# Kernel optimization log

Measured on AMD Instinct MI355X. Metric: run time of the kernel, lower is better.

Reference implementation:

```python
import jax, jax.numpy as jnp
import numpy as np

NODES_PER_GRAPH = 64
HIDDEN = 128
NUM_LAYERS = 4
NUM_CLASSES = 32
EPS = 1e-5


def fully_adjacent_edges(n, num_batches):
    # block-diagonal fully connected edges: within each graph, all (src, dst) pairs
    offs = jnp.arange(num_batches, dtype=jnp.int32) * n          # [G]
    a = jnp.arange(n, dtype=jnp.int32)
    src = jnp.broadcast_to(offs[:, None, None] + a[None, :, None], (num_batches, n, n)).reshape(-1)
    dst = jnp.broadcast_to(offs[:, None, None] + a[None, None, :], (num_batches, n, n)).reshape(-1)
    return jnp.stack([src, dst])  # [2, G*n*n]


def gcn_conv(h, edge_index, W, b, num_nodes):
    loops = jnp.arange(num_nodes, dtype=edge_index.dtype)
    src = jnp.concatenate([edge_index[0], loops])
    dst = jnp.concatenate([edge_index[1], loops])
    deg = jax.ops.segment_sum(jnp.ones_like(dst, dtype=h.dtype), dst, num_segments=num_nodes)
    dinv = jnp.where(deg > 0, jax.lax.rsqrt(deg), 0.0)
    hw = h @ W                                         # [N, H]
    norm = dinv[src] * dinv[dst]                       # [E+N]
    msg = hw[src] * norm[:, None]                      # [E+N, H] (dominant traffic)
    return jax.ops.segment_sum(msg, dst, num_segments=num_nodes) + b


def layer_norm(h, g, b):
    mu = jnp.mean(h, axis=-1, keepdims=True)
    var = jnp.mean(jnp.square(h - mu), axis=-1, keepdims=True)
    return (h - mu) * jax.lax.rsqrt(var + EPS) * g + b


def setup_inputs() -> dict:
    key = jax.random.key(0)
    ks = jax.random.split(key, 8)
    G, n = 256, NODES_PER_GRAPH
    N = G * n
    E = 262144
    x = jax.random.randint(ks[0], (N, 2), 0, NUM_CLASSES, dtype=jnp.int32)
    edge_index = jax.random.randint(ks[1], (2, E), 0, N, dtype=jnp.int32)
    batch = (jnp.arange(N, dtype=jnp.int32) // n).astype(jnp.int32)
    s = 1.0 / np.sqrt(HIDDEN)
    return {
        "x": x,
        "edge_index": edge_index,
        "batch": batch,
        "class_emb": jax.random.normal(ks[2], (NUM_CLASSES, HIDDEN), jnp.float32) * 0.02,
        "neigh_emb": jax.random.normal(ks[3], (NUM_CLASSES, HIDDEN), jnp.float32) * 0.02,
        "Ws": jax.random.normal(ks[4], (NUM_LAYERS, HIDDEN, HIDDEN), jnp.float32) * s,
        "bs": jnp.zeros((NUM_LAYERS, HIDDEN), jnp.float32),
        "ln_g": jnp.ones((NUM_LAYERS, HIDDEN), jnp.float32),
        "ln_b": jnp.zeros((NUM_LAYERS, HIDDEN), jnp.float32),
        "out_W": jax.random.normal(ks[5], (HIDDEN, NUM_CLASSES), jnp.float32) * s,
        "out_b": jnp.zeros((NUM_CLASSES,), jnp.float32),
    }


def reference(x, edge_index, batch, class_emb, neigh_emb, Ws, bs, ln_g, ln_b, out_W, out_b):
    N = x.shape[0]
    G = N // NODES_PER_GRAPH
    h = class_emb[x[:, 0]] + neigh_emb[x[:, 1]]          # embedding sum  [N, H]
    fa_edges = fully_adjacent_edges(NODES_PER_GRAPH, G)  # use_fully_adj=True -> last layer
    for i in range(NUM_LAYERS):
        ei = fa_edges if (i + 1 == NUM_LAYERS) else edge_index
        h_new = jax.nn.relu(gcn_conv(h, ei, Ws[i], bs[i], N))
        h = layer_norm(h + h_new, ln_g[i], ln_b[i])
    roots = jnp.arange(G) * NODES_PER_GRAPH              # root_mask: node 0 of each graph
    return h[roots] @ out_W + out_b                      # [G, NUM_CLASSES]
```

## Files before the change

kernel.cpp:

```cpp
#include <hip/hip_runtime.h>

#define NN 16384
#define EE 262144
#define HH 128
#define GG 256
#define NPG 64
#define ELLW 64

__global__ __launch_bounds__(256) void k_ell(const int* __restrict__ ei,
                                             int* __restrict__ cnt, int* __restrict__ col) {
  int e = blockIdx.x * 256 + threadIdx.x;
  int d = ei[EE + e];
  int s = atomicAdd(&cnt[d], 1);
  if (s < ELLW) col[d * ELLW + s] = ei[e];
}

__device__ __forceinline__ void gemm32(const float (*Al)[132], float* Wl,
                                       const float* __restrict__ W, float* __restrict__ C,
                                       int rbase, int tid) {
  int cg = (tid & 31) * 4;
  int rg = (tid >> 5) * 2;
  float acc[2][4];
#pragma unroll
  for (int i = 0; i < 2; ++i)
#pragma unroll
    for (int j = 0; j < 4; ++j) acc[i][j] = 0.f;
  for (int kc = 0; kc < 4; ++kc) {
    int k0 = kc * 32;
#pragma unroll
    for (int i = 0; i < 2; ++i) {
      int f = tid + 512 * i;
      int kk = f >> 5, q = f & 31;
      *(float4*)&Wl[kk * 128 + q * 4] = *(const float4*)&W[(k0 + kk) * HH + q * 4];
    }
    __syncthreads();
#pragma unroll
    for (int kk = 0; kk < 32; kk += 4) {
      float av[2][4], wv_[4][4];
#pragma unroll
      for (int i = 0; i < 2; ++i) *(float4*)av[i] = *(const float4*)&Al[rg + i][k0 + kk];
#pragma unroll
      for (int j = 0; j < 4; ++j) *(float4*)wv_[j] = *(const float4*)&Wl[(kk + j) * 128 + cg];
#pragma unroll
      for (int j = 0; j < 4; ++j)
#pragma unroll
        for (int i = 0; i < 2; ++i)
#pragma unroll
          for (int c = 0; c < 4; ++c) acc[i][c] = fmaf(av[i][j], wv_[j][c], acc[i][c]);
    }
    __syncthreads();
  }
#pragma unroll
  for (int i = 0; i < 2; ++i) {
    float4 o; o.x = acc[i][0]; o.y = acc[i][1]; o.z = acc[i][2]; o.w = acc[i][3];
    *(float4*)&C[(rbase + rg + i) * HH + cg] = o;
  }
}

__global__ __launch_bounds__(512) void k_emb_gemm(const int* __restrict__ x,
    const float* __restrict__ ce, const float* __restrict__ ne, const float* __restrict__ W,
    const int* __restrict__ cnt, float* __restrict__ h, float* __restrict__ hw,
    float* __restrict__ dinv) {
  __shared__ __align__(16) float Wl[32 * 128];
  __shared__ __align__(16) float Al[32][132];
  int tid = threadIdx.x;
  int rbase = blockIdx.x * 32;
#pragma unroll
  for (int u = 0; u < 2; ++u) {
    int idx = tid + 512 * u;
    int r = idx >> 5, q = idx & 31;
    int2 cls = ((const int2*)x)[rbase + r];
    float4 a = ((const float4*)ce)[cls.x * 32 + q];
    float4 b = ((const float4*)ne)[cls.y * 32 + q];
    float4 o; o.x = a.x + b.x; o.y = a.y + b.y; o.z = a.z + b.z; o.w = a.w + b.w;
    *(float4*)&Al[r][q * 4] = o;
    ((float4*)h)[(rbase + r) * 32 + q] = o;
  }
  if (tid < 32) dinv[rbase + tid] = rsqrtf((float)(cnt[rbase + tid] + 1));
  gemm32(Al, Wl, W, hw, rbase, tid);
}

__global__ __launch_bounds__(512) void k_agg_gemm(const float* __restrict__ hwin,
    float* __restrict__ h, const int* __restrict__ col, const int* __restrict__ cnt,
    const float* __restrict__ dinv, const float* __restrict__ bias,
    const float* __restrict__ g, const float* __restrict__ bln,
    const float* __restrict__ W, float* __restrict__ hwout) {
  __shared__ __align__(16) float Wl[32 * 128];
  __shared__ __align__(16) float Al[32][132];
  int tid = threadIdx.x, wv = tid >> 6, lane = tid & 63;
  int rbase = blockIdx.x * 32;
  const float2* hw2 = (const float2*)hwin;
  float2* h2 = (float2*)h;
  int d = lane * 2;
  float2 b2 = *(const float2*)&bias[d];
  float2 gg = *(const float2*)&g[d];
  float2 bb = *(const float2*)&bln[d];
#pragma unroll 1
  for (int i = 0; i < 4; ++i) {
    int n = rbase + wv * 4 + i;
    float dn = dinv[n];
    float2 sv = hw2[n * 64 + lane];
    float a0x = sv.x * dn * dn, a0y = sv.y * dn * dn;
    float a1x = 0.f, a1y = 0.f, a2x = 0.f, a2y = 0.f, a3x = 0.f, a3y = 0.f;
    int m = cnt[n]; m = m > ELLW ? ELLW : m;
    int cl = 0; float dv = 0.f;
    if (lane < m) { cl = col[n * ELLW + lane]; dv = dinv[cl]; }
    int j = 0;
    for (; j + 4 <= m; j += 4) {
      int s0 = __shfl(cl, j),     s1 = __shfl(cl, j + 1);
      int s2 = __shfl(cl, j + 2), s3 = __shfl(cl, j + 3);
      float n0 = __shfl(dv, j) * dn,     n1 = __shfl(dv, j + 1) * dn;
      float n2 = __shfl(dv, j + 2) * dn, n3 = __shfl(dv, j + 3) * dn;
      float2 v0 = hw2[s0 * 64 + lane];
      float2 v1 = hw2[s1 * 64 + lane];
      float2 v2 = hw2[s2 * 64 + lane];
      float2 v3 = hw2[s3 * 64 + lane];
      a0x = fmaf(v0.x, n0, a0x); a0y = fmaf(v0.y, n0, a0y);
      a1x = fmaf(v1.x, n1, a1x); a1y = fmaf(v1.y, n1, a1y);
      a2x = fmaf(v2.x, n2, a2x); a2y = fmaf(v2.y, n2, a2y);
      a3x = fmaf(v3.x, n3, a3x); a3y = fmaf(v3.y, n3, a3y);
    }
    for (; j < m; ++j) {
      int s0 = __shfl(cl, j); float n0 = __shfl(dv, j) * dn;
      float2 v0 = hw2[s0 * 64 + lane];
      a0x = fmaf(v0.x, n0, a0x); a0y = fmaf(v0.y, n0, a0y);
    }
    float accx = (a0x + a1x) + (a2x + a3x);
    float accy = (a0y + a1y) + (a2y + a3y);
    float hnx = fmaxf(accx + b2.x, 0.f), hny = fmaxf(accy + b2.y, 0.f);
    float2 hv = h2[n * 64 + lane];
    float rx = hv.x + hnx, ry = hv.y + hny;
    float s1 = rx + ry, s2 = rx * rx + ry * ry;
#pragma unroll
    for (int o = 1; o < 64; o <<= 1) { s1 += __shfl_xor(s1, o); s2 += __shfl_xor(s2, o); }
    float mu = s1 * (1.f / 128.f);
    float var = s2 * (1.f / 128.f) - mu * mu;
    float rstd = rsqrtf(var + 1e-5f);
    float2 o2;
    o2.x = (rx - mu) * rstd * gg.x + bb.x;
    o2.y = (ry - mu) * rstd * gg.y + bb.y;
    h2[n * 64 + lane] = o2;
    *(float2*)&Al[wv * 4 + i][2 * lane] = o2;
  }
  gemm32(Al, Wl, W, hwout, rbase, tid);
}

__global__ __launch_bounds__(256) void k_fa_out(const float* __restrict__ hw, float* __restrict__ h,
    const float* __restrict__ bias, const float* __restrict__ g, const float* __restrict__ bln,
    const float* __restrict__ oW, const float* __restrict__ ob, float* __restrict__ out) {
  __shared__ float tmp[256];
  __shared__ float gsum[128];
  __shared__ float part[8][32];
  int gph = blockIdx.x;
  int tid = threadIdx.x;
  int d = tid & 127, half = tid >> 7;
  const float* hwbase = hw + gph * NPG * HH;
  float s = 0.f;
#pragma unroll
  for (int r = 0; r < 32; ++r) s += hwbase[(half * 32 + r) * HH + d];
  tmp[tid] = s;
  __syncthreads();
  if (tid < 128) gsum[tid] = tmp[tid] + tmp[tid + 128];
  __syncthreads();
  int wv = tid >> 6, lane = tid & 63;
  const float inv65 = 1.0f / 65.0f;
  float2 gs = *(const float2*)&gsum[lane * 2];
  float2 b2 = *(const float2*)&bias[lane * 2];
  float2 gg = *(const float2*)&g[lane * 2];
  float2 bb = *(const float2*)&bln[lane * 2];
  __syncthreads();
  for (int ni = wv; ni < NPG; ni += 4) {
    int n = gph * NPG + ni;
    float2 hwv = ((const float2*)hw)[n * 64 + lane];
    float ax = fmaxf((gs.x + hwv.x) * inv65 + b2.x, 0.f);
    float ay = fmaxf((gs.y + hwv.y) * inv65 + b2.y, 0.f);
    float2 hv = ((float2*)h)[n * 64 + lane];
    float rx = hv.x + ax, ry = hv.y + ay;
    float s1 = rx + ry, s2 = rx * rx + ry * ry;
#pragma unroll
    for (int o = 1; o < 64; o <<= 1) { s1 += __shfl_xor(s1, o); s2 += __shfl_xor(s2, o); }
    float mu = s1 * (1.f / 128.f);
    float var = s2 * (1.f / 128.f) - mu * mu;
    float rstd = rsqrtf(var + 1e-5f);
    float2 o2;
    o2.x = (rx - mu) * rstd * gg.x + bb.x;
    o2.y = (ry - mu) * rstd * gg.y + bb.y;
    if (ni == 0) { tmp[lane * 2] = o2.x; tmp[lane * 2 + 1] = o2.y; }
  }
  __syncthreads();
  int c = tid & 31, seg = tid >> 5;
  float p = 0.f;
#pragma unroll
  for (int k = 0; k < 16; ++k) p = fmaf(tmp[seg * 16 + k], oW[(seg * 16 + k) * 32 + c], p);
  part[seg][c] = p;
  __syncthreads();
  if (tid < 32) {
    float so = ob[tid];
#pragma unroll
    for (int i = 0; i < 8; ++i) so += part[i][tid];
    out[gph * 32 + tid] = so;
  }
}

extern "C" void kernel_launch(void* const* d_in, const int* in_sizes, int n_in,
                              void* d_out, int out_size, void* d_ws, size_t ws_size,
                              hipStream_t stream) {
  const int*   x  = (const int*)d_in[0];
  const int*   ei = (const int*)d_in[1];
  const float* ce = (const float*)d_in[3];
  const float* ne = (const float*)d_in[4];
  const float* Ws = (const float*)d_in[5];
  const float* bs = (const float*)d_in[6];
  const float* lg = (const float*)d_in[7];
  const float* lb = (const float*)d_in[8];
  const float* oW = (const float*)d_in[9];
  const float* ob = (const float*)d_in[10];
  float* out = (float*)d_out;

  float* h    = (float*)d_ws;
  float* hwA  = h + NN * HH;
  float* hwB  = hwA + NN * HH;
  int*   cnt  = (int*)(hwB + NN * HH);
  float* dinv = (float*)(cnt + NN);
  int*   col  = (int*)(dinv + NN);

  hipMemsetAsync(cnt, 0, NN * sizeof(int), stream);
  k_ell<<<EE / 256, 256, 0, stream>>>(ei, cnt, col);
  k_emb_gemm<<<NN / 32, 512, 0, stream>>>(x, ce, ne, Ws, cnt, h, hwA, dinv);
  k_agg_gemm<<<NN / 32, 512, 0, stream>>>(hwA, h, col, cnt, dinv,
                                          bs, lg, lb, Ws + 1 * HH * HH, hwB);
  k_agg_gemm<<<NN / 32, 512, 0, stream>>>(hwB, h, col, cnt, dinv,
                                          bs + HH, lg + HH, lb + HH, Ws + 2 * HH * HH, hwA);
  k_agg_gemm<<<NN / 32, 512, 0, stream>>>(hwA, h, col, cnt, dinv,
                                          bs + 2 * HH, lg + 2 * HH, lb + 2 * HH, Ws + 3 * HH * HH, hwB);
  k_fa_out<<<GG, 256, 0, stream>>>(hwB, h, bs + 3 * HH, lg + 3 * HH, lb + 3 * HH, oW, ob, out);
}
```

Baseline: 204.2 us.

## Reorder layers to aggregate-then-GEMM and compute final layer only for roots

Each GCN layer now aggregates neighbour features first and then multiplies by W, using (A·H)·W in place of A·(H·W). The GEMM epilogue applies bias, ReLU, residual and LayerNorm, so one kernel per layer produces h directly and the separate hw buffers go away. Layer 0 gathers embeddings on the fly instead of materialising them. The fully-adjacent last layer is computed only for root nodes, as a per-graph mean times W3, which skips the GEMM and LayerNorm for all other nodes. dinv is recomputed from cnt with rsqrt instead of being stored. The cost is extra embedding gathers in layer 0 and extra cnt reads for the rsqrt recomputation.

```diff
diff --git a/kernel.cpp b/kernel.cpp
--- a/kernel.cpp
+++ b/kernel.cpp
@@ -15,12 +15,11 @@
   if (s < ELLW) col[d * ELLW + s] = ei[e];
 }
 
-__device__ __forceinline__ void gemm32(const float (*Al)[132], float* Wl,
-                                       const float* __restrict__ W, float* __restrict__ C,
-                                       int rbase, int tid) {
+__device__ __forceinline__ void gemm32_acc(const float (*Al)[132], float* Wl,
+                                           const float* __restrict__ W, int tid,
+                                           float acc[2][4]) {
   int cg = (tid & 31) * 4;
   int rg = (tid >> 5) * 2;
-  float acc[2][4];
 #pragma unroll
   for (int i = 0; i < 2; ++i)
 #pragma unroll
@@ -50,155 +49,223 @@
     }
     __syncthreads();
   }
+}
+
+__device__ __forceinline__ void epilogue_store(float acc[2][4], const float4 res[2],
+    const float* __restrict__ bias, const float* __restrict__ g, const float* __restrict__ bln,
+    float* __restrict__ h_out, int rbase, int tid) {
+  int cg = (tid & 31) * 4;
+  int rg = (tid >> 5) * 2;
+  float4 b4 = *(const float4*)&bias[cg];
+  float4 g4 = *(const float4*)&g[cg];
+  float4 l4 = *(const float4*)&bln[cg];
 #pragma unroll
   for (int i = 0; i < 2; ++i) {
-    float4 o; o.x = acc[i][0]; o.y = acc[i][1]; o.z = acc[i][2]; o.w = acc[i][3];
-    *(float4*)&C[(rbase + rg + i) * HH + cg] = o;
-  }
-}
-
-__global__ __launch_bounds__(512) void k_emb_gemm(const int* __restrict__ x,
-    const float* __restrict__ ce, const float* __restrict__ ne, const float* __restrict__ W,
-    const int* __restrict__ cnt, float* __restrict__ h, float* __restrict__ hw,
-    float* __restrict__ dinv) {
-  __shared__ __align__(16) float Wl[32 * 128];
-  __shared__ __align__(16) float Al[32][132];
-  int tid = threadIdx.x;
-  int rbase = blockIdx.x * 32;
-#pragma unroll
-  for (int u = 0; u < 2; ++u) {
-    int idx = tid + 512 * u;
-    int r = idx >> 5, q = idx & 31;
-    int2 cls = ((const int2*)x)[rbase + r];
-    float4 a = ((const float4*)ce)[cls.x * 32 + q];
-    float4 b = ((const float4*)ne)[cls.y * 32 + q];
-    float4 o; o.x = a.x + b.x; o.y = a.y + b.y; o.z = a.z + b.z; o.w = a.w + b.w;
-    *(float4*)&Al[r][q * 4] = o;
-    ((float4*)h)[(rbase + r) * 32 + q] = o;
-  }
-  if (tid < 32) dinv[rbase + tid] = rsqrtf((float)(cnt[rbase + tid] + 1));
-  gemm32(Al, Wl, W, hw, rbase, tid);
-}
-
-__global__ __launch_bounds__(512) void k_agg_gemm(const float* __restrict__ hwin,
-    float* __restrict__ h, const int* __restrict__ col, const int* __restrict__ cnt,
-    const float* __restrict__ dinv, const float* __restrict__ bias,
-    const float* __restrict__ g, const float* __restrict__ bln,
-    const float* __restrict__ W, float* __restrict__ hwout) {
+    int n = rbase + rg + i;
+    float vx = fmaxf(acc[i][0] + b4.x, 0.f) + res[i].x;
+    float vy = fmaxf(acc[i][1] + b4.y, 0.f) + res[i].y;
+    float vz = fmaxf(acc[i][2] + b4.z, 0.f) + res[i].z;
+    float vw = fmaxf(acc[i][3] + b4.w, 0.f) + res[i].w;
+    float s1 = (vx + vy) + (vz + vw);
+    float s2 = (vx * vx + vy * vy) + (vz * vz + vw * vw);
+#pragma unroll
+    for (int o = 1; o < 32; o <<= 1) { s1 += __shfl_xor(s1, o); s2 += __shfl_xor(s2, o); }
+    float mu = s1 * (1.f / 128.f);
+    float var = s2 * (1.f / 128.f) - mu * mu;
+    float rstd = rsqrtf(var + 1e-5f);
+    float4 o4;
+    o4.x = (vx - mu) * rstd * g4.x + l4.x;
+    o4.y = (vy - mu) * rstd * g4.y + l4.y;
+    o4.z = (vz - mu) * rstd * g4.z + l4.z;
+    o4.w = (vw - mu) * rstd * g4.w + l4.w;
+    *(float4*)&h_out[n * HH + cg] = o4;
+  }
+}
+
+__global__ __launch_bounds__(512) void k_layer0(const int* __restrict__ x,
+    const float* __restrict__ ce, const float* __restrict__ ne,
+    const int* __restrict__ col, const int* __restrict__ cnt,
+    const float* __restrict__ bias, const float* __restrict__ g, const float* __restrict__ bln,
+    const float* __restrict__ W, float* __restrict__ h_out) {
   __shared__ __align__(16) float Wl[32 * 128];
   __shared__ __align__(16) float Al[32][132];
   int tid = threadIdx.x, wv = tid >> 6, lane = tid & 63;
   int rbase = blockIdx.x * 32;
-  const float2* hw2 = (const float2*)hwin;
-  float2* h2 = (float2*)h;
-  int d = lane * 2;
-  float2 b2 = *(const float2*)&bias[d];
-  float2 gg = *(const float2*)&g[d];
-  float2 bb = *(const float2*)&bln[d];
+  const int2* x2 = (const int2*)x;
+  const float2* ce2 = (const float2*)ce;
+  const float2* ne2 = (const float2*)ne;
 #pragma unroll 1
   for (int i = 0; i < 4; ++i) {
     int n = rbase + wv * 4 + i;
-    float dn = dinv[n];
-    float2 sv = hw2[n * 64 + lane];
-    float a0x = sv.x * dn * dn, a0y = sv.y * dn * dn;
+    int cn_ = cnt[n];
+    float dn = rsqrtf((float)cn_ + 1.0f);
+    int2 cc = x2[n];
+    float2 e0 = ce2[cc.x * 64 + lane];
+    float2 e1 = ne2[cc.y * 64 + lane];
+    float svx = e0.x + e1.x, svy = e0.y + e1.y;
+    float a0x = svx * dn * dn, a0y = svy * dn * dn;
     float a1x = 0.f, a1y = 0.f, a2x = 0.f, a2y = 0.f, a3x = 0.f, a3y = 0.f;
-    int m = cnt[n]; m = m > ELLW ? ELLW : m;
-    int cl = 0; float dv = 0.f;
-    if (lane < m) { cl = col[n * ELLW + lane]; dv = dinv[cl]; }
+    int m = cn_ > ELLW ? ELLW : cn_;
+    int pc = 0; float dv = 0.f;
+    if (lane < m) {
+      int cl = col[n * ELLW + lane];
+      int2 cs = x2[cl];
+      pc = cs.x | (cs.y << 16);
+      dv = rsqrtf((float)cnt[cl] + 1.0f);
+    }
     int j = 0;
     for (; j + 4 <= m; j += 4) {
-      int s0 = __shfl(cl, j),     s1 = __shfl(cl, j + 1);
-      int s2 = __shfl(cl, j + 2), s3 = __shfl(cl, j + 3);
+      int p0 = __shfl(pc, j),     p1 = __shfl(pc, j + 1);
+      int p2 = __shfl(pc, j + 2), p3 = __shfl(pc, j + 3);
       float n0 = __shfl(dv, j) * dn,     n1 = __shfl(dv, j + 1) * dn;
       float n2 = __shfl(dv, j + 2) * dn, n3 = __shfl(dv, j + 3) * dn;
-      float2 v0 = hw2[s0 * 64 + lane];
-      float2 v1 = hw2[s1 * 64 + lane];
-      float2 v2 = hw2[s2 * 64 + lane];
-      float2 v3 = hw2[s3 * 64 + lane];
-      a0x = fmaf(v0.x, n0, a0x); a0y = fmaf(v0.y, n0, a0y);
-      a1x = fmaf(v1.x, n1, a1x); a1y = fmaf(v1.y, n1, a1y);
-      a2x = fmaf(v2.x, n2, a2x); a2y = fmaf(v2.y, n2, a2y);
-      a3x = fmaf(v3.x, n3, a3x); a3y = fmaf(v3.y, n3, a3y);
+      float2 r0 = ce2[(p0 & 0xffff) * 64 + lane], q0 = ne2[(p0 >> 16) * 64 + lane];
+      float2 r1 = ce2[(p1 & 0xffff) * 64 + lane], q1 = ne2[(p1 >> 16) * 64 + lane];
+      float2 r2 = ce2[(p2 & 0xffff) * 64 + lane], q2 = ne2[(p2 >> 16) * 64 + lane];
+      float2 r3 = ce2[(p3 & 0xffff) * 64 + lane], q3 = ne2[(p3 >> 16) * 64 + lane];
+      a0x = fmaf(r0.x + q0.x, n0, a0x); a0y = fmaf(r0.y + q0.y, n0, a0y);
+      a1x = fmaf(r1.x + q1.x, n1, a1x); a1y = fmaf(r1.y + q1.y, n1, a1y);
+      a2x = fmaf(r2.x + q2.x, n2, a2x); a2y = fmaf(r2.y + q2.y, n2, a2y);
+      a3x = fmaf(r3.x + q3.x, n3, a3x); a3y = fmaf(r3.y + q3.y, n3, a3y);
     }
     for (; j < m; ++j) {
-      int s0 = __shfl(cl, j); float n0 = __shfl(dv, j) * dn;
-      float2 v0 = hw2[s0 * 64 + lane];
-      a0x = fmaf(v0.x, n0, a0x); a0y = fmaf(v0.y, n0, a0y);
-    }
-    float accx = (a0x + a1x) + (a2x + a3x);
-    float accy = (a0y + a1y) + (a2y + a3y);
-    float hnx = fmaxf(accx + b2.x, 0.f), hny = fmaxf(accy + b2.y, 0.f);
-    float2 hv = h2[n * 64 + lane];
-    float rx = hv.x + hnx, ry = hv.y + hny;
-    float s1 = rx + ry, s2 = rx * rx + ry * ry;
+      int p0 = __shfl(pc, j); float n0 = __shfl(dv, j) * dn;
+      float2 r0 = ce2[(p0 & 0xffff) * 64 + lane], q0 = ne2[(p0 >> 16) * 64 + lane];
+      a0x = fmaf(r0.x + q0.x, n0, a0x); a0y = fmaf(r0.y + q0.y, n0, a0y);
+    }
+    Al[wv * 4 + i][2 * lane]     = (a0x + a1x) + (a2x + a3x);
+    Al[wv * 4 + i][2 * lane + 1] = (a0y + a1y) + (a2y + a3y);
+  }
+  float acc[2][4];
+  gemm32_acc(Al, Wl, W, tid, acc);
+  int cg = (tid & 31) * 4, rg = (tid >> 5) * 2;
+  const float4* ce4 = (const float4*)ce;
+  const float4* ne4 = (const float4*)ne;
+  float4 res[2];
+#pragma unroll
+  for (int i = 0; i < 2; ++i) {
+    int2 cc = x2[rbase + rg + i];
+    float4 a = ce4[cc.x * 32 + (cg >> 2)];
+    float4 b = ne4[cc.y * 32 + (cg >> 2)];
+    res[i].x = a.x + b.x; res[i].y = a.y + b.y; res[i].z = a.z + b.z; res[i].w = a.w + b.w;
+  }
+  epilogue_store(acc, res, bias, g, bln, h_out, rbase, tid);
+}
+
+__global__ __launch_bounds__(512) void k_layer(const float* __restrict__ h_in,
+    float* __restrict__ h_out, const int* __restrict__ col, const int* __restrict__ cnt,
+    const float* __restrict__ bias, const float* __restrict__ g, const float* __restrict__ bln,
+    const float* __restrict__ W) {
+  __shared__ __align__(16) float Wl[32 * 128];
+  __shared__ __align__(16) float Al[32][132];
+  int tid = threadIdx.x, wv = tid >> 6, lane = tid & 63;
+  int c4 = lane & 31, half = lane >> 5;
+  int rbase = blockIdx.x * 32;
+  const float4* h4 = (const float4*)h_in;
+#pragma unroll 1
+  for (int i = 0; i < 4; ++i) {
+    int n = rbase + wv * 4 + i;
+    int cn_ = cnt[n];
+    float dn = rsqrtf((float)cn_ + 1.0f);
+    int m = cn_ > ELLW ? ELLW : cn_;
+    int cl = n; float dv = 0.f;
+    if (lane < m) { cl = col[n * ELLW + lane]; dv = rsqrtf((float)cnt[cl] + 1.0f); }
+    float4 a0; a0.x = 0.f; a0.y = 0.f; a0.z = 0.f; a0.w = 0.f;
+    float4 a1; a1.x = 0.f; a1.y = 0.f; a1.z = 0.f; a1.w = 0.f;
+    int pairs = (m + 1) >> 1;
+    int t = 0;
+    for (; t + 2 <= pairs; t += 2) {
+      int e0 = 2 * t + half, e1 = 2 * (t + 1) + half;
+      int s0 = __shfl(cl, e0); float q0 = __shfl(dv, e0) * dn;
+      int s1 = __shfl(cl, e1); float q1 = __shfl(dv, e1) * dn;
+      float4 v0 = h4[s0 * 32 + c4];
+      float4 v1 = h4[s1 * 32 + c4];
+      a0.x = fmaf(v0.x, q0, a0.x); a0.y = fmaf(v0.y, q0, a0.y);
+      a0.z = fmaf(v0.z, q0, a0.z); a0.w = fmaf(v0.w, q0, a0.w);
+      a1.x = fmaf(v1.x, q1, a1.x); a1.y = fmaf(v1.y, q1, a1.y);
+      a1.z = fmaf(v1.z, q1, a1.z); a1.w = fmaf(v1.w, q1, a1.w);
+    }
+    for (; t < pairs; ++t) {
+      int e0 = 2 * t + half;
+      int s0 = __shfl(cl, e0); float q0 = __shfl(dv, e0) * dn;
+      float4 v0 = h4[s0 * 32 + c4];
+      a0.x = fmaf(v0.x, q0, a0.x); a0.y = fmaf(v0.y, q0, a0.y);
+      a0.z = fmaf(v0.z, q0, a0.z); a0.w = fmaf(v0.w, q0, a0.w);
+    }
+    float4 tt;
+    tt.x = a0.x + a1.x; tt.y = a0.y + a1.y; tt.z = a0.z + a1.z; tt.w = a0.w + a1.w;
+    tt.x += __shfl_xor(tt.x, 32); tt.y += __shfl_xor(tt.y, 32);
+    tt.z += __shfl_xor(tt.z, 32); tt.w += __shfl_xor(tt.w, 32);
+    float4 sv = h4[n * 32 + c4];
+    float w2 = dn * dn;
+    tt.x = fmaf(sv.x, w2, tt.x); tt.y = fmaf(sv.y, w2, tt.y);
+    tt.z = fmaf(sv.z, w2, tt.z); tt.w = fmaf(sv.w, w2, tt.w);
+    if (half == 0) *(float4*)&Al[wv * 4 + i][c4 * 4] = tt;
+  }
+  float acc[2][4];
+  gemm32_acc(Al, Wl, W, tid, acc);
+  int cg = (tid & 31) * 4, rg = (tid >> 5) * 2;
+  float4 res[2];
+#pragma unroll
+  for (int i = 0; i < 2; ++i) res[i] = *(const float4*)&h_in[(rbase + rg + i) * HH + cg];
+  epilogue_store(acc, res, bias, g, bln, h_out, rbase, tid);
+}
+
+__global__ __launch_bounds__(256) void k_fa_root(const float* __restrict__ hA,
+    const float* __restrict__ W3, const float* __restrict__ b3,
+    const float* __restrict__ g3, const float* __restrict__ l3,
+    const float* __restrict__ oW, const float* __restrict__ ob, float* __restrict__ out) {
+  __shared__ float s_sum[256];
+  __shared__ float s_a[128];
+  __shared__ float s_hr[128];
+  __shared__ float s_r[128];
+  __shared__ float s_y[128];
+  __shared__ float s_red[2];
+  int gph = blockIdx.x, tid = threadIdx.x;
+  const float* base = hA + gph * NPG * HH;
+  int c = tid & 127, half = tid >> 7;
+  float s = 0.f;
+#pragma unroll
+  for (int r = 0; r < 32; ++r) s += base[(half * 32 + r) * HH + c];
+  s_sum[tid] = s;
+  __syncthreads();
+  if (tid < 128) {
+    float gs = s_sum[tid] + s_sum[tid + 128];
+    float hr = base[tid];
+    s_hr[tid] = hr;
+    s_a[tid] = (gs + hr) * (1.0f / 65.0f);
+  }
+  __syncthreads();
+  if (tid < 128) {
+    float acc = 0.f;
+#pragma unroll 8
+    for (int k = 0; k < 128; ++k) acc = fmaf(s_a[k], W3[k * HH + tid], acc);
+    float t = fmaxf(acc + b3[tid], 0.f);
+    s_r[tid] = s_hr[tid] + t;
+  }
+  __syncthreads();
+  if (tid < 64) {
+    float v0 = s_r[tid], v1 = s_r[tid + 64];
+    float s1 = v0 + v1, s2 = v0 * v0 + v1 * v1;
 #pragma unroll
     for (int o = 1; o < 64; o <<= 1) { s1 += __shfl_xor(s1, o); s2 += __shfl_xor(s2, o); }
-    float mu = s1 * (1.f / 128.f);
-    float var = s2 * (1.f / 128.f) - mu * mu;
-    float rstd = rsqrtf(var + 1e-5f);
-    float2 o2;
-    o2.x = (rx - mu) * rstd * gg.x + bb.x;
-    o2.y = (ry - mu) * rstd * gg.y + bb.y;
-    h2[n * 64 + lane] = o2;
-    *(float2*)&Al[wv * 4 + i][2 * lane] = o2;
-  }
-  gemm32(Al, Wl, W, hwout, rbase, tid);
-}
-
-__global__ __launch_bounds__(256) void k_fa_out(const float* __restrict__ hw, float* __restrict__ h,
-    const float* __restrict__ bias, const float* __restrict__ g, const float* __restrict__ bln,
-    const float* __restrict__ oW, const float* __restrict__ ob, float* __restrict__ out) {
-  __shared__ float tmp[256];
-  __shared__ float gsum[128];
-  __shared__ float part[8][32];
-  int gph = blockIdx.x;
-  int tid = threadIdx.x;
-  int d = tid & 127, half = tid >> 7;
-  const float* hwbase = hw + gph * NPG * HH;
-  float s = 0.f;
-#pragma unroll
-  for (int r = 0; r < 32; ++r) s += hwbase[(half * 32 + r) * HH + d];
-  tmp[tid] = s;
-  __syncthreads();
-  if (tid < 128) gsum[tid] = tmp[tid] + tmp[tid + 128];
-  __syncthreads();
-  int wv = tid >> 6, lane = tid & 63;
-  const float inv65 = 1.0f / 65.0f;
-  float2 gs = *(const float2*)&gsum[lane * 2];
-  float2 b2 = *(const float2*)&bias[lane * 2];
-  float2 gg = *(const float2*)&g[lane * 2];
-  float2 bb = *(const float2*)&bln[lane * 2];
-  __syncthreads();
-  for (int ni = wv; ni < NPG; ni += 4) {
-    int n = gph * NPG + ni;
-    float2 hwv = ((const float2*)hw)[n * 64 + lane];
-    float ax = fmaxf((gs.x + hwv.x) * inv65 + b2.x, 0.f);
-    float ay = fmaxf((gs.y + hwv.y) * inv65 + b2.y, 0.f);
-    float2 hv = ((float2*)h)[n * 64 + lane];
-    float rx = hv.x + ax, ry = hv.y + ay;
-    float s1 = rx + ry, s2 = rx * rx + ry * ry;
-#pragma unroll
-    for (int o = 1; o < 64; o <<= 1) { s1 += __shfl_xor(s1, o); s2 += __shfl_xor(s2, o); }
-    float mu = s1 * (1.f / 128.f);
-    float var = s2 * (1.f / 128.f) - mu * mu;
-    float rstd = rsqrtf(var + 1e-5f);
-    float2 o2;
-    o2.x = (rx - mu) * rstd * gg.x + bb.x;
-    o2.y = (ry - mu) * rstd * gg.y + bb.y;
-    if (ni == 0) { tmp[lane * 2] = o2.x; tmp[lane * 2 + 1] = o2.y; }
-  }
-  __syncthreads();
-  int c = tid & 31, seg = tid >> 5;
-  float p = 0.f;
-#pragma unroll
-  for (int k = 0; k < 16; ++k) p = fmaf(tmp[seg * 16 + k], oW[(seg * 16 + k) * 32 + c], p);
-  part[seg][c] = p;
+    if (tid == 0) {
+      float mu = s1 * (1.f / 128.f);
+      float var = s2 * (1.f / 128.f) - mu * mu;
+      s_red[0] = mu; s_red[1] = rsqrtf(var + 1e-5f);
+    }
+  }
+  __syncthreads();
+  if (tid < 128) {
+    float mu = s_red[0], rstd = s_red[1];
+    s_y[tid] = (s_r[tid] - mu) * rstd * g3[tid] + l3[tid];
+  }
   __syncthreads();
   if (tid < 32) {
-    float so = ob[tid];
-#pragma unroll
-    for (int i = 0; i < 8; ++i) so += part[i][tid];
-    out[gph * 32 + tid] = so;
+    float acc = ob[tid];
+#pragma unroll 8
+    for (int k = 0; k < 128; ++k) acc = fmaf(s_y[k], oW[k * 32 + tid], acc);
+    out[gph * 32 + tid] = acc;
   }
 }
 
@@ -217,21 +284,19 @@
   const float* ob = (const float*)d_in[10];
   float* out = (float*)d_out;
 
-  float* h    = (float*)d_ws;
-  float* hwA  = h + NN * HH;
-  float* hwB  = hwA + NN * HH;
-  int*   cnt  = (int*)(hwB + NN * HH);
-  float* dinv = (float*)(cnt + NN);
-  int*   col  = (int*)(dinv + NN);
+  float* hA  = (float*)d_ws;
+  float* hB  = hA + NN * HH;
+  int*   cnt = (int*)(hB + NN * HH);
+  int*   col = cnt + NN;
 
   hipMemsetAsync(cnt, 0, NN * sizeof(int), stream);
   k_ell<<<EE / 256, 256, 0, stream>>>(ei, cnt, col);
-  k_emb_gemm<<<NN / 32, 512, 0, stream>>>(x, ce, ne, Ws, cnt, h, hwA, dinv);
-  k_agg_gemm<<<NN / 32, 512, 0, stream>>>(hwA, h, col, cnt, dinv,
-                                          bs, lg, lb, Ws + 1 * HH * HH, hwB);
-  k_agg_gemm<<<NN / 32, 512, 0, stream>>>(hwB, h, col, cnt, dinv,
-                                          bs + HH, lg + HH, lb + HH, Ws + 2 * HH * HH, hwA);
-  k_agg_gemm<<<NN / 32, 512, 0, stream>>>(hwA, h, col, cnt, dinv,
-                                          bs + 2 * HH, lg + 2 * HH, lb + 2 * HH, Ws + 3 * HH * HH, hwB);
-  k_fa_out<<<GG, 256, 0, stream>>>(hwB, h, bs + 3 * HH, lg + 3 * HH, lb + 3 * HH, oW, ob, out);
-}
+  k_layer0<<<NN / 32, 512, 0, stream>>>(x, ce, ne, col, cnt,
+                                        bs, lg, lb, Ws, hA);
+  k_layer<<<NN / 32, 512, 0, stream>>>(hA, hB, col, cnt,
+                                       bs + HH, lg + HH, lb + HH, Ws + HH * HH);
+  k_layer<<<NN / 32, 512, 0, stream>>>(hB, hA, col, cnt,
+                                       bs + 2 * HH, lg + 2 * HH, lb + 2 * HH, Ws + 2 * HH * HH);
+  k_fa_root<<<GG, 256, 0, stream>>>(hA, Ws + 3 * HH * HH, bs + 3 * HH,
+                                    lg + 3 * HH, lb + 3 * HH, oW, ob, out);
+}
```

New measurement: 188.8 us. -7.6%, faster.
